# Performance work log

Hardware: AMD Instinct MI355X
Metric: run time of the kernel (lower is better)

Reference implementation:

```python
import jax, jax.numpy as jnp
import numpy as np

K = 31          # local attention window (odd)
PAD = (K - 1) // 2
G = 8           # heads / groups
MC = 48         # model_complexity (attention out_features)
OF = 88         # output_features
BN_EPS = 1e-5


def conv2d(x, w, b):
    # x: [B,C,H,W], w: [O,I,3,3], 'SAME' == padding=1 for stride-1 3x3
    y = jax.lax.conv_general_dilated(x, w, (1, 1), 'SAME',
                                     dimension_numbers=('NCHW', 'OIHW', 'NCHW'))
    return y + b[None, :, None, None]


def bn(x, g, b, m, v):
    # inference-mode BatchNorm2d over channel dim of NCHW
    return (x - m[None, :, None, None]) * (g[None, :, None, None] /
           jnp.sqrt(v[None, :, None, None] + BN_EPS)) + b[None, :, None, None]


def maxpool_w2(x):
    # MaxPool2d((1,2)): pool width (freq) by 2
    return jax.lax.reduce_window(x, -jnp.inf, jax.lax.max,
                                 (1, 1, 1, 2), (1, 1, 1, 2), 'VALID')


def setup_inputs() -> dict:
    key = jax.random.key(0)
    ks = jax.random.split(key, 24)
    B, T, F = 8, 2560, 229
    C1, C2 = OF // 16, OF // 8          # 5, 11
    freq_feats = C2 * (F // 2 // 2)      # 11 * 57 = 627
    s = lambda k, shp, sc=0.05: jax.random.normal(k, shp, dtype=jnp.float32) * sc
    inp = {
        'spec':   jax.random.normal(ks[0], (B, T, F), dtype=jnp.float32),
        'c1_w': s(ks[1], (C1, 1, 3, 3)),  'c1_b': s(ks[2], (C1,)),
        'bn1_g': jnp.ones((C1,)), 'bn1_b': jnp.zeros((C1,)),
        'bn1_m': jnp.zeros((C1,)), 'bn1_v': jnp.ones((C1,)),
        'c2_w': s(ks[3], (C1, C1, 3, 3)), 'c2_b': s(ks[4], (C1,)),
        'bn2_g': jnp.ones((C1,)), 'bn2_b': jnp.zeros((C1,)),
        'bn2_m': jnp.zeros((C1,)), 'bn2_v': jnp.ones((C1,)),
        'c3_w': s(ks[5], (C2, C1, 3, 3)), 'c3_b': s(ks[6], (C2,)),
        'bn3_g': jnp.ones((C2,)), 'bn3_b': jnp.zeros((C2,)),
        'bn3_m': jnp.zeros((C2,)), 'bn3_v': jnp.ones((C2,)),
        'fc_w': s(ks[7], (OF, freq_feats)), 'fc_b': s(ks[8], (OF,)),
        'wq': s(ks[9], (MC, OF)), 'wk': s(ks[10], (MC, OF)), 'wv': s(ks[11], (MC, OF)),
        'rel': jax.random.normal(ks[12], (1, MC, K), dtype=jnp.float32),
        'ln_g': jnp.ones((MC,)), 'ln_b': jnp.zeros((MC,)),
        'lin_w': s(ks[13], (OF, MC)), 'lin_b': s(ks[14], (OF,)),
    }
    return inp


def reference(spec, c1_w, c1_b, bn1_g, bn1_b, bn1_m, bn1_v,
              c2_w, c2_b, bn2_g, bn2_b, bn2_m, bn2_v,
              c3_w, c3_b, bn3_g, bn3_b, bn3_m, bn3_v,
              fc_w, fc_b, wq, wk, wv, rel, ln_g, ln_b, lin_w, lin_b):
    B, T, F = spec.shape
    # ---- ConvStack (eval mode: BN uses running stats, dropout = identity) ----
    x = spec[:, None]                                  # [B,1,T,F]
    x = jax.nn.relu(bn(conv2d(x, c1_w, c1_b), bn1_g, bn1_b, bn1_m, bn1_v))
    x = jax.nn.relu(bn(conv2d(x, c2_w, c2_b), bn2_g, bn2_b, bn2_m, bn2_v))
    x = maxpool_w2(x)                                  # F -> F//2
    x = jax.nn.relu(bn(conv2d(x, c3_w, c3_b), bn3_g, bn3_b, bn3_m, bn3_v))
    x = maxpool_w2(x)                                  # F//2 -> F//4
    x = jnp.transpose(x, (0, 2, 1, 3)).reshape(B, T, -1)  # [B,T,C2*(F//4)]
    x = x @ fc_w.T + fc_b                              # [B,T,OF]

    # ---- MutliHeadAttention1D: local windowed attention via unfold ----
    q = x @ wq.T                                       # [B,T,MC]
    xp = jnp.pad(x, ((0, 0), (PAD, PAD), (0, 0)))
    k = xp @ wk.T                                      # [B,T+K-1,MC]
    v = xp @ wv.T
    idx = jnp.arange(T)[:, None] + jnp.arange(K)[None, :]   # [T,K]
    kw = jnp.transpose(k[:, idx], (0, 1, 3, 2)) + rel        # [B,T,MC,K]
    vw = jnp.transpose(v[:, idx], (0, 1, 3, 2))              # [B,T,MC,K]
    Dh = MC // G
    kw = kw.reshape(B, T, G, Dh, K)
    vw = vw.reshape(B, T, G, Dh, K)
    qh = q.reshape(B, T, G, Dh, 1)
    energy = (qh * kw).sum(-2, keepdims=True)          # [B,T,G,1,K]
    attn = jax.nn.softmax(energy, axis=-1)
    out = (attn * vw).sum(-1).reshape(B, T, MC)        # [B,T,MC]
    a = attn.squeeze(3)                                # [B,T,G,K]

    # ---- LayerNorm + Linear + sigmoid ----
    mu = out.mean(-1, keepdims=True)
    var = jnp.mean((out - mu) ** 2, axis=-1, keepdims=True)
    h = (out - mu) / jnp.sqrt(var + 1e-5) * ln_g + ln_b
    frame_pred = jax.nn.sigmoid(h @ lin_w.T + lin_b)   # [B,T,OF]
    return frame_pred, a
```

## Files before the change

kernel.cpp:

```cpp
#include <hip/hip_runtime.h>
#include <hip/hip_bf16.h>
#include <math.h>

#define B_    8
#define T_    2560
#define F_    229
#define C1_   5
#define C2_   11
#define W1_   114
#define W2_   57
#define KP_   640
#define OF_   88
#define MC_   48
#define G_    8
#define DH_   6
#define K_    31
#define PAD_  15
#define BN_EPS 1e-5f
#define LN_EPS 1e-5f
#define TS_   10
#define TT_   16

typedef __attribute__((ext_vector_type(8))) short short8;
typedef __attribute__((ext_vector_type(4))) float f32x4;
typedef _Float16 h2 __attribute__((ext_vector_type(2)));
typedef __fp16 fp16x2 __attribute__((ext_vector_type(2)));

static inline int cdiv(int a, int b) { return (a + b - 1) / b; }

union H2U { h2 h; unsigned u; };

__device__ inline h2 uph2(unsigned u) { H2U x; x.u = u; return x.h; }
__device__ inline unsigned packh2(float lo, float hi) {
    H2U x;
    x.h.x = (_Float16)lo;
    x.h.y = (_Float16)hi;
    return x.u;
}

#if __has_builtin(__builtin_amdgcn_cvt_pkrtz)
__device__ inline unsigned pkrtz(float a, float b) {
    union { fp16x2 v; unsigned u; } x;
    x.v = __builtin_amdgcn_cvt_pkrtz(a, b);
    return x.u;
}
#else
__device__ inline unsigned pkrtz(float a, float b) { return packh2(a, b); }
#endif

#if __has_builtin(__builtin_amdgcn_fdot2)
#define FDOT2(a, b, c) __builtin_amdgcn_fdot2((a), (b), (c), false)
#else
__device__ inline float FDOT2(h2 a, h2 b, float c) {
    return fmaf((float)a.x, (float)b.x, fmaf((float)a.y, (float)b.y, c));
}
#endif

__global__ __launch_bounds__(640, 8) void conv123_kernel(
        const float* __restrict__ spec,
        const float* __restrict__ c1w, const float* __restrict__ c1b,
        const float* __restrict__ g1, const float* __restrict__ b1,
        const float* __restrict__ m1, const float* __restrict__ v1,
        const float* __restrict__ c2w, const float* __restrict__ c2b,
        const float* __restrict__ g2, const float* __restrict__ b2,
        const float* __restrict__ m2, const float* __restrict__ v2,
        const float* __restrict__ c3w, const float* __restrict__ c3b,
        const float* __restrict__ g3, const float* __restrict__ b3,
        const float* __restrict__ m3, const float* __restrict__ v3,
        __hip_bfloat16* __restrict__ x3out) {
    __shared__ __align__(16) ushort x1t[70 * 240];
    __shared__ __align__(16) ushort x2u[7216];
    __shared__ __align__(16) unsigned w1p[60];
    __shared__ __align__(16) unsigned w2p[300];
    __shared__ __align__(16) unsigned w3p[660];
    __shared__ float scl1[5], shf1[5], scl2[5], shf2[5], scl3[11], shf3[11];
    int t0 = blockIdx.x * TS_;
    int b = blockIdx.y;
    int tid = threadIdx.x;

    if (tid < 15) {
        int co = tid / 3, dt = tid % 3;
        const float* wp = c1w + co * 9 + dt * 3;
        unsigned* dst = &w1p[tid * 4];
        dst[0] = packh2(wp[0], wp[1]);
        dst[1] = packh2(wp[2], 0.f);
        dst[2] = packh2(0.f, wp[0]);
        dst[3] = packh2(wp[1], wp[2]);
    }
    for (int i = tid; i < 75; i += 640) {
        int r = i % 15;
        const float* wp = c2w + (i / 15) * 45 + (r / 3) * 9 + (r % 3) * 3;
        unsigned* dst = &w2p[i * 4];
        dst[0] = packh2(wp[0], wp[1]);
        dst[1] = packh2(wp[2], 0.f);
        dst[2] = packh2(0.f, wp[0]);
        dst[3] = packh2(wp[1], wp[2]);
    }
    for (int i = tid; i < 165; i += 640) {
        int r = i % 15;
        const float* wp = c3w + (i / 15) * 45 + (r / 3) * 9 + (r % 3) * 3;
        unsigned* dst = &w3p[i * 4];
        dst[0] = packh2(wp[0], wp[1]);
        dst[1] = packh2(wp[2], 0.f);
        dst[2] = packh2(0.f, wp[0]);
        dst[3] = packh2(wp[1], wp[2]);
    }
    if (tid < 5) {
        float s = g1[tid] * rsqrtf(v1[tid] + BN_EPS);
        scl1[tid] = s;
        shf1[tid] = (c1b[tid] - m1[tid]) * s + b1[tid];
    }
    if (tid >= 64 && tid < 69) {
        int c = tid - 64;
        float s = g2[c] * rsqrtf(v2[c] + BN_EPS);
        scl2[c] = s;
        shf2[c] = (c2b[c] - m2[c]) * s + b2[c];
    }
    if (tid >= 128 && tid < 139) {
        int c = tid - 128;
        float s = g3[c] * rsqrtf(v3[c] + BN_EPS);
        scl3[c] = s;
        shf3[c] = (c3b[c] - m3[c]) * s + b3[c];
    }
    {
        const float* sb = spec + (size_t)b * T_ * F_;
        for (int i = tid; i < 16 * 120; i += 640) {
            int row = i / 120;
            int pr = i - row * 120;
            int t = t0 - 3 + row;
            int c = 2 * pr - 4;
            float va = 0.f, vb = 0.f;
            if (t >= 0 && t < T_) {
                const float* rp = sb + (size_t)t * F_;
                if ((unsigned)c < 229u) va = rp[c];
                if ((unsigned)(c + 1) < 229u) vb = rp[c + 1];
            }
            *(unsigned*)&x2u[row * 240 + 2 * pr] = packh2(va, vb);
        }
        if (tid == 0) {
            uint4 z = {0u, 0u, 0u, 0u};
            *(uint4*)&x2u[7200] = z;
            *(uint4*)&x2u[7208] = z;
        }
    }
    __syncthreads();

    if (tid < 580) {
        int co = tid / 116;
        int rem = tid - co * 116;
        int q = rem >> 2;
        int rg = rem & 3;
        int rlo = rg * 3 + (rg ? 1 : 0);
        const unsigned* wb = &w1p[co * 12];
        uint4 wv0 = *(const uint4*)wb;
        uint4 wv1 = *(const uint4*)(wb + 4);
        uint4 wv2 = *(const uint4*)(wb + 8);
        h2 A1[3] = {uph2(wv0.x), uph2(wv1.x), uph2(wv2.x)};
        h2 B1[3] = {uph2(wv0.y), uph2(wv1.y), uph2(wv2.y)};
        h2 C1v[3] = {uph2(wv0.z), uph2(wv1.z), uph2(wv2.z)};
        h2 D1[3] = {uph2(wv0.w), uph2(wv1.w), uph2(wv2.w)};
        h2 X[6][5];
        const ushort* sp = x2u + 8 * q;
#pragma unroll
        for (int s = 0; s < 6; ++s) {
            const ushort* p = sp + (rlo + s) * 240;
            uint4 xq = *(const uint4*)p;
            unsigned xr = *(const unsigned*)(p + 8);
            X[s][0] = uph2(xq.x); X[s][1] = uph2(xq.y);
            X[s][2] = uph2(xq.z); X[s][3] = uph2(xq.w);
            X[s][4] = uph2(xr);
        }
        float s1 = scl1[co], h1 = shf1[co];
        int c0 = 8 * q - 3;
#pragma unroll
        for (int k = 0; k < 4; ++k) {
            int rr1 = rlo + k;
            int t = t0 - 2 + rr1;
            bool vt = (t >= 0 && t < T_);
            float y[8] = {0.f, 0.f, 0.f, 0.f, 0.f, 0.f, 0.f, 0.f};
#pragma unroll
            for (int dt = 0; dt < 3; ++dt) {
#pragma unroll
                for (int l = 0; l < 4; ++l) {
                    y[2 * l] = FDOT2(X[k + dt][l + 1], B1[dt],
                               FDOT2(X[k + dt][l], A1[dt], y[2 * l]));
                    y[2 * l + 1] = FDOT2(X[k + dt][l + 1], D1[dt],
                                   FDOT2(X[k + dt][l], C1v[dt], y[2 * l + 1]));
                }
            }
            unsigned pk[4];
#pragma unroll
            for (int m = 0; m < 4; ++m) {
                float ya = fmaxf(fmaf(y[2 * m], s1, h1), 0.f);
                float yb = fmaxf(fmaf(y[2 * m + 1], s1, h1), 0.f);
                ya = (vt && (c0 + 2 * m) >= 0) ? ya : 0.f;
                yb = (vt && (c0 + 2 * m + 1) >= 0) ? yb : 0.f;
                pk[m] = pkrtz(ya, yb);
            }
            uint4 pw = {pk[0], pk[1], pk[2], pk[3]};
            *(uint4*)&x1t[(rr1 * 5 + co) * 240 + 8 * q] = pw;
        }
    }
    if (tid < 70) {
        uint4 z = {0u, 0u, 0u, 0u};
        *(uint4*)&x1t[tid * 240 + 232] = z;
    }
    __syncthreads();

    if (tid < 580) {
        int co = tid / 116;
        int rem = tid - co * 116;
        int q2 = rem >> 2;
        int rg = rem & 3;
        int rlo = rg * 3;
        float aE[3][4], aO[3][4];
#pragma unroll
        for (int i = 0; i < 3; ++i)
#pragma unroll
            for (int l = 0; l < 4; ++l) { aE[i][l] = 0.f; aO[i][l] = 0.f; }
        const ushort* px = x1t + 8 * q2;
        for (int ci = 0; ci < 5; ++ci) {
            const unsigned* wb = &w2p[(co * 5 + ci) * 12];
            uint4 wv0 = *(const uint4*)wb;
            uint4 wv1 = *(const uint4*)(wb + 4);
            uint4 wv2 = *(const uint4*)(wb + 8);
            h2 A[3] = {uph2(wv0.x), uph2(wv1.x), uph2(wv2.x)};
            h2 Bb[3] = {uph2(wv0.y), uph2(wv1.y), uph2(wv2.y)};
            h2 Cc[3] = {uph2(wv0.z), uph2(wv1.z), uph2(wv2.z)};
            h2 Dd[3] = {uph2(wv0.w), uph2(wv1.w), uph2(wv2.w)};
#pragma unroll
            for (int k = 0; k < 5; ++k) {
                const ushort* p = px + ((rlo + k) * 5 + ci) * 240;
                uint4 xq = *(const uint4*)p;
                unsigned xr = *(const unsigned*)(p + 8);
                h2 X[5] = {uph2(xq.x), uph2(xq.y), uph2(xq.z), uph2(xq.w), uph2(xr)};
#pragma unroll
                for (int dt = 0; dt < 3; ++dt) {
                    int lr = k - dt;
                    if (lr >= 0 && lr < 3) {
#pragma unroll
                        for (int l = 0; l < 4; ++l) {
                            aE[lr][l] = FDOT2(X[l + 1], Bb[dt],
                                        FDOT2(X[l], A[dt], aE[lr][l]));
                            aO[lr][l] = FDOT2(X[l + 1], Dd[dt],
                                        FDOT2(X[l], Cc[dt], aO[lr][l]));
                        }
                    }
                }
            }
        }
        float s = scl2[co], sh = shf2[co];
#pragma unroll
        for (int lr = 0; lr < 3; ++lr) {
            int r = rlo + lr;
            int t = t0 - 1 + r;
            bool vt = (t >= 0 && t < T_);
            float yv[4];
#pragma unroll
            for (int l = 0; l < 4; ++l) {
                int j = 4 * q2 - 1 + l;
                float y = fmaxf(fmaxf(fmaf(aE[lr][l], s, sh), 0.f),
                                fmaxf(fmaf(aO[lr][l], s, sh), 0.f));
                yv[l] = (vt && j >= 0 && j < 114) ? y : 0.f;
            }
            uint2 pw;
            pw.x = pkrtz(yv[0], yv[1]);
            pw.y = pkrtz(yv[2], yv[3]);
            *(uint2*)&x2u[(r * 5 + co) * 120 + 4 * q2] = pw;
        }
    }
    __syncthreads();

    if (tid < 495) {
        int co = tid / 45;
        int rem = tid - co * 45;
        int pq = rem / 3;
        int rg = rem - pq * 3;
        int rlo = rg * 3;
        float aE[4][4], aO[4][4];
#pragma unroll
        for (int i = 0; i < 4; ++i)
#pragma unroll
            for (int l = 0; l < 4; ++l) { aE[i][l] = 0.f; aO[i][l] = 0.f; }
        const ushort* px = x2u + 8 * pq;
        for (int ci = 0; ci < 5; ++ci) {
            const unsigned* wb = &w3p[(co * 5 + ci) * 12];
            uint4 wv0 = *(const uint4*)wb;
            uint4 wv1 = *(const uint4*)(wb + 4);
            uint4 wv2 = *(const uint4*)(wb + 8);
            h2 A[3] = {uph2(wv0.x), uph2(wv1.x), uph2(wv2.x)};
            h2 Bb[3] = {uph2(wv0.y), uph2(wv1.y), uph2(wv2.y)};
            h2 Cc[3] = {uph2(wv0.z), uph2(wv1.z), uph2(wv2.z)};
            h2 Dd[3] = {uph2(wv0.w), uph2(wv1.w), uph2(wv2.w)};
#pragma unroll
            for (int k = 0; k < 6; ++k) {
                const ushort* p = px + ((rlo + k) * 5 + ci) * 120;
                uint4 xq = *(const uint4*)p;
                unsigned xr = *(const unsigned*)(p + 8);
                h2 X[5] = {uph2(xq.x), uph2(xq.y), uph2(xq.z), uph2(xq.w), uph2(xr)};
#pragma unroll
                for (int dt = 0; dt < 3; ++dt) {
                    int lr = k - dt;
                    if (lr >= 0 && lr < 4) {
#pragma unroll
                        for (int l = 0; l < 4; ++l) {
                            aE[lr][l] = FDOT2(X[l + 1], Bb[dt],
                                        FDOT2(X[l], A[dt], aE[lr][l]));
                            aO[lr][l] = FDOT2(X[l + 1], Dd[dt],
                                        FDOT2(X[l], Cc[dt], aO[lr][l]));
                        }
                    }
                }
            }
        }
        float s = scl3[co], sh = shf3[co];
#pragma unroll
        for (int lr = 0; lr < 4; ++lr) {
            int rout = rlo + lr;
            size_t rowbase = (size_t)(b * T_ + t0 + rout) * KP_ + co * 57;
#pragma unroll
            for (int l = 0; l < 4; ++l) {
                int j = 4 * pq + l;
                if (j < 57) {
                    float y = fmaxf(fmaxf(fmaf(aE[lr][l], s, sh), 0.f),
                                    fmaxf(fmaf(aO[lr][l], s, sh), 0.f));
                    x3out[rowbase + j] = __float2bfloat16(y);
                }
            }
        }
    } else {
        __hip_bfloat16 z = __float2bfloat16(0.f);
        for (int i = tid - 495; i < TS_ * 13; i += 145) {
            int r = i / 13, c = 627 + (i - (i / 13) * 13);
            x3out[(size_t)(b * T_ + t0 + r) * KP_ + c] = z;
        }
    }
}

__global__ __launch_bounds__(256) void wprime_kernel(const float* __restrict__ fc_w,
        const float* __restrict__ fc_b, const float* __restrict__ wq,
        const float* __restrict__ wk, const float* __restrict__ wv,
        __hip_bfloat16* __restrict__ wp, float* __restrict__ bp) {
    int idx = blockIdx.x * 256 + threadIdx.x;
    if (idx < 144 * KP_) {
        int o = idx / KP_;
        int kk = idx % KP_;
        const float* Wrow = (o < 48) ? (wq + o * 88)
                          : (o < 96) ? (wk + (o - 48) * 88) : (wv + (o - 96) * 88);
        float s = 0.f;
        if (kk < 627)
            for (int i = 0; i < 88; ++i) s = fmaf(Wrow[i], fc_w[(size_t)i * 627 + kk], s);
        wp[idx] = __float2bfloat16(s);
    } else if (idx < 144 * KP_ + 144) {
        int o = idx - 144 * KP_;
        const float* Wrow = (o < 48) ? (wq + o * 88)
                          : (o < 96) ? (wk + (o - 48) * 88) : (wv + (o - 96) * 88);
        float s = 0.f;
        for (int i = 0; i < 88; ++i) s = fmaf(Wrow[i], fc_b[i], s);
        bp[o] = s;
    }
}

__global__ __launch_bounds__(256) void fc_qkv_mfma_kernel(
        const __hip_bfloat16* __restrict__ X, const __hip_bfloat16* __restrict__ Wp,
        const float* __restrict__ bp, float* __restrict__ Q) {
    int tid = threadIdx.x;
    int lane = tid & 63;
    int gw = blockIdx.x * 4 + (tid >> 6);
    int mtile = gw / 3;
    int nthird = gw % 3;
    const short* Xs = (const short*)X;
    const short* Ws = (const short*)Wp;
    int klane = (lane >> 4) * 8;
    const short* xrow = Xs + (size_t)(mtile * 16 + (lane & 15)) * KP_ + klane;
    const short* wrow = Ws + (size_t)(nthird * 48 + (lane & 15)) * KP_ + klane;
    f32x4 acc0 = {0.f, 0.f, 0.f, 0.f}, acc1 = acc0, acc2 = acc0;
#pragma unroll 4
    for (int kt = 0; kt < 20; ++kt) {
        short8 a = *(const short8*)(xrow + kt * 32);
        short8 b0 = *(const short8*)(wrow + kt * 32);
        short8 b1 = *(const short8*)(wrow + 16 * KP_ + kt * 32);
        short8 b2 = *(const short8*)(wrow + 32 * KP_ + kt * 32);
        acc0 = __builtin_amdgcn_mfma_f32_16x16x32_bf16(a, b0, acc0, 0, 0, 0);
        acc1 = __builtin_amdgcn_mfma_f32_16x16x32_bf16(a, b1, acc1, 0, 0, 0);
        acc2 = __builtin_amdgcn_mfma_f32_16x16x32_bf16(a, b2, acc2, 0, 0, 0);
    }
    int r0 = mtile * 16 + (lane >> 4) * 4;
    int col = lane & 15;
    f32x4 accs[3] = {acc0, acc1, acc2};
#pragma unroll
    for (int nt = 0; nt < 3; ++nt) {
        int o = nthird * 48 + nt * 16 + col;
        float bias = bp[o];
#pragma unroll
        for (int rg = 0; rg < 4; ++rg)
            Q[(size_t)(r0 + rg) * 144 + o] = accs[nt][rg] + bias;
    }
}

__global__ __launch_bounds__(256) void attn_ln_kernel(const float* __restrict__ Q,
        const float* __restrict__ rel, const float* __restrict__ lng,
        const float* __restrict__ lnb, const float* __restrict__ lw,
        const float* __restrict__ lb, float* __restrict__ fp,
        float* __restrict__ aout) {
    __shared__ float smem[6088];
    __shared__ float mus[TT_], rss[TT_];
    float* kvt = smem;
    float* relT = smem + 4600;
    int b = blockIdx.y;
    int t0 = blockIdx.x * TT_;
    int tid = threadIdx.x;
    int h = tid & 1;
    int p = tid >> 1;
    int g = p & 7;
    int tl = p >> 3;
    for (int i = tid; i < 46 * 48; i += 256) {
        int row = i / 48, c2 = i % 48;
        int t = t0 - 15 + row;
        float2 v = {0.f, 0.f};
        if (t >= 0 && t < T_)
            v = *(const float2*)&Q[((size_t)b * T_ + t) * 144 + 48 + 2 * c2];
        *(float2*)&kvt[row * 100 + 2 * c2] = v;
    }
    for (int i = tid; i < 31 * 48; i += 256) {
        int kp = i / 48, j = i % 48;
        relT[i] = rel[j * 31 + kp];
    }
    const float* qg = &Q[((size_t)b * T_ + t0 + tl) * 144 + g * 6];
    float2 q01 = *(const float2*)qg;
    float2 q23 = *(const float2*)(qg + 2);
    float2 q45 = *(const float2*)(qg + 4);
    __syncthreads();
    float e[16];
    float m_h = -1e30f;
#pragma unroll
    for (int i = 0; i < 16; ++i) {
        int kp = 2 * i + h;
        if (kp < 31) {
            const float* kr = &kvt[(tl + kp) * 100 + g * 6];
            const float* rr = &relT[kp * 48 + g * 6];
            float2 k01 = *(const float2*)kr;
            float2 k23 = *(const float2*)(kr + 2);
            float2 k45 = *(const float2*)(kr + 4);
            float2 r01 = *(const float2*)rr;
            float2 r23 = *(const float2*)(rr + 2);
            float2 r45 = *(const float2*)(rr + 4);
            float s = fmaf(q01.x, k01.x + r01.x,
                      fmaf(q01.y, k01.y + r01.y,
                      fmaf(q23.x, k23.x + r23.x,
                      fmaf(q23.y, k23.y + r23.y,
                      fmaf(q45.x, k45.x + r45.x,
                           q45.y * (k45.y + r45.y))))));
            e[i] = s;
            m_h = fmaxf(m_h, s);
        }
    }
    float M = fmaxf(m_h, __shfl_xor(m_h, 1));
    float s_h = 0.f;
    float o0 = 0, o1 = 0, o2 = 0, o3 = 0, o4 = 0, o5 = 0;
#pragma unroll
    for (int i = 0; i < 16; ++i) {
        int kp = 2 * i + h;
        if (kp < 31) {
            float a = __expf(e[i] - M);
            e[i] = a;
            s_h += a;
            const float* vr = &kvt[(tl + kp) * 100 + 48 + g * 6];
            float2 v01 = *(const float2*)vr;
            float2 v23 = *(const float2*)(vr + 2);
            float2 v45 = *(const float2*)(vr + 4);
            o0 = fmaf(a, v01.x, o0); o1 = fmaf(a, v01.y, o1);
            o2 = fmaf(a, v23.x, o2); o3 = fmaf(a, v23.y, o3);
            o4 = fmaf(a, v45.x, o4); o5 = fmaf(a, v45.y, o5);
        }
    }
    float sum = s_h + __shfl_xor(s_h, 1);
    float inv = 1.f / sum;
    float t0s = o0 + __shfl_xor(o0, 1);
    float t1s = o1 + __shfl_xor(o1, 1);
    float t2s = o2 + __shfl_xor(o2, 1);
    float t3s = o3 + __shfl_xor(o3, 1);
    float t4s = o4 + __shfl_xor(o4, 1);
    float t5s = o5 + __shfl_xor(o5, 1);
    __syncthreads();
    float* abuf = smem;
    float* xr = smem + 3968;
#pragma unroll
    for (int i = 0; i < 16; ++i) {
        int kp = 2 * i + h;
        if (kp < 31) abuf[p * 31 + kp] = e[i] * inv;
    }
    if (h == 0) {
        float* xp = &xr[tl * 48 + g * 6];
        xp[0] = t0s * inv; xp[1] = t1s * inv; xp[2] = t2s * inv;
        xp[3] = t3s * inv; xp[4] = t4s * inv; xp[5] = t5s * inv;
    }
    __syncthreads();
    size_t base = ((size_t)b * T_ + t0) * 248;
    for (int i = tid; i < 992; i += 256) {
        float4 v = *(const float4*)&abuf[4 * i];
        *(float4*)&aout[base + 4 * i] = v;
    }
    if (tid < TT_) {
        const float* row = &xr[tid * 48];
        float s = 0.f;
        for (int c = 0; c < 48; ++c) s += row[c];
        float mu = s * (1.f / 48.f);
        float v2 = 0.f;
        for (int c = 0; c < 48; ++c) { float d = row[c] - mu; v2 = fmaf(d, d, v2); }
        mus[tid] = mu;
        rss[tid] = rsqrtf(v2 * (1.f / 48.f) + LN_EPS);
    }
    __syncthreads();
    for (int i = tid; i < TT_ * 48; i += 256) {
        int r = i / 48, c = i % 48;
        xr[i] = fmaf((xr[i] - mus[r]) * rss[r], lng[c], lnb[c]);
    }
    __syncthreads();
    size_t obase = ((size_t)b * T_ + t0) * 88;
    for (int i = tid; i < TT_ * 88; i += 256) {
        int o = i % 88, r = i / 88;
        const float* xp = &xr[r * 48];
        const float* wpp = &lw[o * 48];
        float s = lb[o];
#pragma unroll
        for (int c = 0; c < 48; c += 4) {
            float4 xv = *(const float4*)&xp[c];
            float4 wv = *(const float4*)&wpp[c];
            s = fmaf(xv.x, wv.x, s);
            s = fmaf(xv.y, wv.y, s);
            s = fmaf(xv.z, wv.z, s);
            s = fmaf(xv.w, wv.w, s);
        }
        fp[obase + i] = 1.f / (1.f + __expf(-s));
    }
}

extern "C" void kernel_launch(void* const* d_in, const int* in_sizes, int n_in,
                              void* d_out, int out_size, void* d_ws, size_t ws_size,
                              hipStream_t stream) {
    const float* spec = (const float*)d_in[0];
    const float* c1_w = (const float*)d_in[1];
    const float* c1_b = (const float*)d_in[2];
    const float* bn1_g = (const float*)d_in[3];
    const float* bn1_b = (const float*)d_in[4];
    const float* bn1_m = (const float*)d_in[5];
    const float* bn1_v = (const float*)d_in[6];
    const float* c2_w = (const float*)d_in[7];
    const float* c2_b = (const float*)d_in[8];
    const float* bn2_g = (const float*)d_in[9];
    const float* bn2_b = (const float*)d_in[10];
    const float* bn2_m = (const float*)d_in[11];
    const float* bn2_v = (const float*)d_in[12];
    const float* c3_w = (const float*)d_in[13];
    const float* c3_b = (const float*)d_in[14];
    const float* bn3_g = (const float*)d_in[15];
    const float* bn3_b = (const float*)d_in[16];
    const float* bn3_m = (const float*)d_in[17];
    const float* bn3_v = (const float*)d_in[18];
    const float* fc_w = (const float*)d_in[19];
    const float* fc_b = (const float*)d_in[20];
    const float* wq = (const float*)d_in[21];
    const float* wk = (const float*)d_in[22];
    const float* wv = (const float*)d_in[23];
    const float* rel = (const float*)d_in[24];
    const float* ln_g = (const float*)d_in[25];
    const float* ln_b = (const float*)d_in[26];
    const float* lin_w = (const float*)d_in[27];
    const float* lin_b = (const float*)d_in[28];

    float* ws = (float*)d_ws;
    __hip_bfloat16* x3bf = (__hip_bfloat16*)ws;
    __hip_bfloat16* wp_bf = (__hip_bfloat16*)(ws + 19000000);
    float* bp = ws + 19100000;
    float* Qb = ws + 23449600;

    float* frame_pred = (float*)d_out;
    float* a_out = frame_pred + (size_t)B_ * T_ * OF_;

    wprime_kernel<<<cdiv(144 * KP_ + 144, 256), 256, 0, stream>>>(fc_w, fc_b, wq, wk, wv,
                                                                  wp_bf, bp);
    conv123_kernel<<<dim3(T_ / TS_, B_), 640, 0, stream>>>(
        spec, c1_w, c1_b, bn1_g, bn1_b, bn1_m, bn1_v,
        c2_w, c2_b, bn2_g, bn2_b, bn2_m, bn2_v,
        c3_w, c3_b, bn3_g, bn3_b, bn3_m, bn3_v, x3bf);
    fc_qkv_mfma_kernel<<<960, 256, 0, stream>>>(x3bf, wp_bf, bp, Qb);
    attn_ln_kernel<<<dim3(T_ / TT_, B_), 256, 0, stream>>>(Qb, rel, ln_g, ln_b, lin_w,
                                                           lin_b, frame_pred, a_out);
}
```

Measured before the change: 304.6 us.

## Fuse QKV projection GEMM into local attention kernel with halo recompute

Removes the separate MFMA QKV projection kernel and computes Q, K, V per attention block directly into shared memory, including the 15-row halo on each side. This eliminates writing and re-reading the fp32 QKV buffer through global memory and one kernel launch. In exchange, K/V rows in the halo are recomputed by neighbouring blocks (48 rows computed for 16 outputs), increasing MFMA work and X reads, and one wave handles an extra column tile, causing imbalance.

```diff
diff --git a/kernel.cpp b/kernel.cpp
--- a/kernel.cpp
+++ b/kernel.cpp
@@ -361,76 +361,114 @@
     }
 }
 
-__global__ __launch_bounds__(256) void fc_qkv_mfma_kernel(
+__global__ __launch_bounds__(256, 4) void attn_fused_kernel(
         const __hip_bfloat16* __restrict__ X, const __hip_bfloat16* __restrict__ Wp,
-        const float* __restrict__ bp, float* __restrict__ Q) {
-    int tid = threadIdx.x;
-    int lane = tid & 63;
-    int gw = blockIdx.x * 4 + (tid >> 6);
-    int mtile = gw / 3;
-    int nthird = gw % 3;
-    const short* Xs = (const short*)X;
-    const short* Ws = (const short*)Wp;
-    int klane = (lane >> 4) * 8;
-    const short* xrow = Xs + (size_t)(mtile * 16 + (lane & 15)) * KP_ + klane;
-    const short* wrow = Ws + (size_t)(nthird * 48 + (lane & 15)) * KP_ + klane;
-    f32x4 acc0 = {0.f, 0.f, 0.f, 0.f}, acc1 = acc0, acc2 = acc0;
-#pragma unroll 4
-    for (int kt = 0; kt < 20; ++kt) {
-        short8 a = *(const short8*)(xrow + kt * 32);
-        short8 b0 = *(const short8*)(wrow + kt * 32);
-        short8 b1 = *(const short8*)(wrow + 16 * KP_ + kt * 32);
-        short8 b2 = *(const short8*)(wrow + 32 * KP_ + kt * 32);
-        acc0 = __builtin_amdgcn_mfma_f32_16x16x32_bf16(a, b0, acc0, 0, 0, 0);
-        acc1 = __builtin_amdgcn_mfma_f32_16x16x32_bf16(a, b1, acc1, 0, 0, 0);
-        acc2 = __builtin_amdgcn_mfma_f32_16x16x32_bf16(a, b2, acc2, 0, 0, 0);
-    }
-    int r0 = mtile * 16 + (lane >> 4) * 4;
-    int col = lane & 15;
-    f32x4 accs[3] = {acc0, acc1, acc2};
-#pragma unroll
-    for (int nt = 0; nt < 3; ++nt) {
-        int o = nthird * 48 + nt * 16 + col;
-        float bias = bp[o];
-#pragma unroll
-        for (int rg = 0; rg < 4; ++rg)
-            Q[(size_t)(r0 + rg) * 144 + o] = accs[nt][rg] + bias;
-    }
-}
-
-__global__ __launch_bounds__(256) void attn_ln_kernel(const float* __restrict__ Q,
-        const float* __restrict__ rel, const float* __restrict__ lng,
-        const float* __restrict__ lnb, const float* __restrict__ lw,
-        const float* __restrict__ lb, float* __restrict__ fp,
-        float* __restrict__ aout) {
-    __shared__ float smem[6088];
+        const float* __restrict__ bp, const float* __restrict__ rel,
+        const float* __restrict__ lng, const float* __restrict__ lnb,
+        const float* __restrict__ lw, const float* __restrict__ lb,
+        float* __restrict__ fp, float* __restrict__ aout) {
+    __shared__ float smem[6856];
     __shared__ float mus[TT_], rss[TT_];
     float* kvt = smem;
     float* relT = smem + 4600;
+    float* qs = smem + 6088;
     int b = blockIdx.y;
     int t0 = blockIdx.x * TT_;
     int tid = threadIdx.x;
+    int lane = tid & 63;
+    int w = tid >> 6;
+
+    for (int i = tid; i < 31 * 48; i += 256) {
+        int kp = i / 48, j = i % 48;
+        relT[i] = rel[j * 31 + kp];
+    }
+
+    {
+        const short* Xs = (const short*)X;
+        const short* Ws = (const short*)Wp;
+        int r16 = lane & 15;
+        int colk = (lane >> 4) * 8;
+        const short *xr0, *xr1, *xr2;
+        {
+            size_t bb = (size_t)b * T_;
+            int t00 = t0 - 15 + r16;
+            int tA0 = t00 < 0 ? 0 : (t00 >= T_ ? T_ - 1 : t00);
+            int t01 = t00 + 16;
+            int tA1 = t01 < 0 ? 0 : (t01 >= T_ ? T_ - 1 : t01);
+            int t02 = t00 + 32;
+            int tA2 = t02 < 0 ? 0 : (t02 >= T_ ? T_ - 1 : t02);
+            xr0 = Xs + (bb + tA0) * KP_ + colk;
+            xr1 = Xs + (bb + tA1) * KP_ + colk;
+            xr2 = Xs + (bb + tA2) * KP_ + colk;
+        }
+        int cnt3 = (w == 0);
+        int n0 = w, n1 = w + 4;
+        const short* wr0 = Ws + (size_t)(n0 * 16 + r16) * KP_ + colk;
+        const short* wr1 = Ws + (size_t)(n1 * 16 + r16) * KP_ + colk;
+        const short* wr2 = Ws + (size_t)(8 * 16 + r16) * KP_ + colk;
+        f32x4 z4 = {0.f, 0.f, 0.f, 0.f};
+        f32x4 acc00 = z4, acc01 = z4, acc02 = z4;
+        f32x4 acc10 = z4, acc11 = z4, acc12 = z4;
+        f32x4 acc20 = z4, acc21 = z4, acc22 = z4;
+#pragma unroll 2
+        for (int kt = 0; kt < 20; ++kt) {
+            short8 a0 = *(const short8*)(xr0 + kt * 32);
+            short8 a1 = *(const short8*)(xr1 + kt * 32);
+            short8 a2 = *(const short8*)(xr2 + kt * 32);
+            short8 bv0 = *(const short8*)(wr0 + kt * 32);
+            short8 bv1 = *(const short8*)(wr1 + kt * 32);
+            acc00 = __builtin_amdgcn_mfma_f32_16x16x32_bf16(a0, bv0, acc00, 0, 0, 0);
+            acc10 = __builtin_amdgcn_mfma_f32_16x16x32_bf16(a1, bv0, acc10, 0, 0, 0);
+            acc20 = __builtin_amdgcn_mfma_f32_16x16x32_bf16(a2, bv0, acc20, 0, 0, 0);
+            acc01 = __builtin_amdgcn_mfma_f32_16x16x32_bf16(a0, bv1, acc01, 0, 0, 0);
+            acc11 = __builtin_amdgcn_mfma_f32_16x16x32_bf16(a1, bv1, acc11, 0, 0, 0);
+            acc21 = __builtin_amdgcn_mfma_f32_16x16x32_bf16(a2, bv1, acc21, 0, 0, 0);
+            if (cnt3) {
+                short8 bv2 = *(const short8*)(wr2 + kt * 32);
+                acc02 = __builtin_amdgcn_mfma_f32_16x16x32_bf16(a0, bv2, acc02, 0, 0, 0);
+                acc12 = __builtin_amdgcn_mfma_f32_16x16x32_bf16(a1, bv2, acc12, 0, 0, 0);
+                acc22 = __builtin_amdgcn_mfma_f32_16x16x32_bf16(a2, bv2, acc22, 0, 0, 0);
+            }
+        }
+        int col = r16;
+        int rg4 = (lane >> 4) * 4;
+        auto writeTile = [&](int M, int N, f32x4 A) {
+            int o = N * 16 + col;
+            float bias = bp[o];
+#pragma unroll
+            for (int i = 0; i < 4; ++i) {
+                int krow = M * 16 + rg4 + i;
+                int t = t0 - 15 + krow;
+                float val = (t >= 0 && t < T_) ? (A[i] + bias) : 0.f;
+                if (o >= 48) {
+                    if (krow < 46) kvt[krow * 100 + (o - 48)] = val;
+                } else if (krow >= 15 && krow < 31) {
+                    qs[(krow - 15) * 48 + o] = val;
+                }
+            }
+        };
+        writeTile(0, n0, acc00);
+        writeTile(1, n0, acc10);
+        writeTile(2, n0, acc20);
+        writeTile(0, n1, acc01);
+        writeTile(1, n1, acc11);
+        writeTile(2, n1, acc21);
+        if (cnt3) {
+            writeTile(0, 8, acc02);
+            writeTile(1, 8, acc12);
+            writeTile(2, 8, acc22);
+        }
+    }
+    __syncthreads();
+
     int h = tid & 1;
     int p = tid >> 1;
     int g = p & 7;
     int tl = p >> 3;
-    for (int i = tid; i < 46 * 48; i += 256) {
-        int row = i / 48, c2 = i % 48;
-        int t = t0 - 15 + row;
-        float2 v = {0.f, 0.f};
-        if (t >= 0 && t < T_)
-            v = *(const float2*)&Q[((size_t)b * T_ + t) * 144 + 48 + 2 * c2];
-        *(float2*)&kvt[row * 100 + 2 * c2] = v;
-    }
-    for (int i = tid; i < 31 * 48; i += 256) {
-        int kp = i / 48, j = i % 48;
-        relT[i] = rel[j * 31 + kp];
-    }
-    const float* qg = &Q[((size_t)b * T_ + t0 + tl) * 144 + g * 6];
+    const float* qg = &qs[tl * 48 + g * 6];
     float2 q01 = *(const float2*)qg;
     float2 q23 = *(const float2*)(qg + 2);
     float2 q45 = *(const float2*)(qg + 4);
-    __syncthreads();
     float e[16];
     float m_h = -1e30f;
 #pragma unroll
@@ -573,7 +611,6 @@
     __hip_bfloat16* x3bf = (__hip_bfloat16*)ws;
     __hip_bfloat16* wp_bf = (__hip_bfloat16*)(ws + 19000000);
     float* bp = ws + 19100000;
-    float* Qb = ws + 23449600;
 
     float* frame_pred = (float*)d_out;
     float* a_out = frame_pred + (size_t)B_ * T_ * OF_;
@@ -584,7 +621,6 @@
         spec, c1_w, c1_b, bn1_g, bn1_b, bn1_m, bn1_v,
         c2_w, c2_b, bn2_g, bn2_b, bn2_m, bn2_v,
         c3_w, c3_b, bn3_g, bn3_b, bn3_m, bn3_v, x3bf);
-    fc_qkv_mfma_kernel<<<960, 256, 0, stream>>>(x3bf, wp_bf, bp, Qb);
-    attn_ln_kernel<<<dim3(T_ / TT_, B_), 256, 0, stream>>>(Qb, rel, ln_g, ln_b, lin_w,
-                                                           lin_b, frame_pred, a_out);
+    attn_fused_kernel<<<dim3(T_ / TT_, B_), 256, 0, stream>>>(
+        x3bf, wp_bf, bp, rel, ln_g, ln_b, lin_w, lin_b, frame_pred, a_out);
 }
```

New measurement: 319.8 us. 1.05x slower.
